# Kernel tuning notes

Measured on AMD Instinct MI355X. Metric: run time of the kernel, lower is better.

## Reference

```python
import jax, jax.numpy as jnp
import numpy as np

T = 1024          # tokens (flattened batch*seq)
H = 1024          # hidden_size
NH = 8            # num_attention_heads
NKV = 4           # num_key_value_heads
HD = H // NH      # head_dim = 128
E = 32            # n_routed_experts
TOPK = 4          # num_experts_per_tok
NG = 8            # n_group
TKG = 4           # topk_group
MI = 512          # moe_intermediate_size
SI = MI * 2       # shared experts intermediate (n_shared_experts=2)
THETA = 10000.0
EPS = 1e-6
RSF = 2.5         # routed_scaling_factor


def setup_inputs() -> dict:
    key = jax.random.key(0)
    ks = jax.random.split(key, 16)
    s = jnp.float32(0.02)
    def nrm(k, shape):
        return jax.random.normal(k, shape, jnp.float32) * s
    return {
        "hidden_states": jax.random.normal(ks[0], (T, H), jnp.float32),
        "position_ids": jnp.arange(T, dtype=jnp.int32),
        "ln1_w": jnp.ones((H,), jnp.float32),
        "ln2_w": jnp.ones((H,), jnp.float32),
        "q_w": nrm(ks[1], (H, H)),            # torch Linear layout [out, in]
        "k_w": nrm(ks[2], (NKV * HD, H)),
        "v_w": nrm(ks[3], (NKV * HD, H)),
        "o_w": nrm(ks[4], (H, H)),
        "router_w": nrm(ks[5], (E, H)),
        "router_bias": jnp.zeros((E,), jnp.float32),  # e_score_correction_bias
        "eg_w": nrm(ks[6], (E, H, MI)),       # expert gate_proj, [E, in, out]
        "eu_w": nrm(ks[7], (E, H, MI)),       # expert up_proj
        "ed_w": nrm(ks[8], (E, MI, H)),       # expert down_proj
        "sg_w": nrm(ks[9], (H, SI)),          # shared experts gate_proj, [in, out]
        "su_w": nrm(ks[10], (H, SI)),
        "sd_w": nrm(ks[11], (SI, H)),
    }


def rmsnorm(x, w):
    var = jnp.mean(x * x, axis=-1, keepdims=True)
    return x * jax.lax.rsqrt(var + EPS) * w


def apply_rope(x, pos):
    # x: [T, heads, HD], non-interleaved (half-rotation)
    half = HD // 2
    inv_freq = 1.0 / (THETA ** (jnp.arange(half, dtype=jnp.float32) / half))
    freqs = pos.astype(jnp.float32)[:, None] * inv_freq[None, :]  # [T, half]
    cos = jnp.cos(freqs)[:, None, :]
    sin = jnp.sin(freqs)[:, None, :]
    x1, x2 = x[..., :half], x[..., half:]
    return jnp.concatenate([x1 * cos - x2 * sin, x2 * cos + x1 * sin], axis=-1)


def attention(h, pos, q_w, k_w, v_w, o_w):
    q = (h @ q_w.T).reshape(T, NH, HD)
    k = (h @ k_w.T).reshape(T, NKV, HD)
    v = (h @ v_w.T).reshape(T, NKV, HD)
    q = apply_rope(q, pos)
    k = apply_rope(k, pos)
    rep = NH // NKV
    k = jnp.repeat(k, rep, axis=1)  # [T, NH, HD]
    v = jnp.repeat(v, rep, axis=1)
    scale = 1.0 / np.sqrt(HD).astype(np.float32)
    scores = jnp.einsum("qhd,khd->hqk", q, k) * scale  # [NH, T, T]
    causal = jnp.tril(jnp.ones((T, T), bool))
    scores = jnp.where(causal[None], scores, jnp.finfo(scores.dtype).min)
    probs = jax.nn.softmax(scores, axis=-1)
    out = jnp.einsum("hqk,khd->qhd", probs, v).reshape(T, H)
    return out @ o_w.T


def router(x, router_w, router_bias):
    logits = x.astype(jnp.float32) @ router_w.T  # [T, E]
    scores = jax.nn.sigmoid(logits)
    sfc = scores + router_bias[None, :]
    # group-limited routing: sum of top-2 per group
    group_scores = jax.lax.top_k(sfc.reshape(T, NG, E // NG), 2)[0].sum(-1)  # [T, NG]
    gidx = jax.lax.top_k(group_scores, TKG)[1]  # [T, TKG]
    gmask = jnp.zeros((T, NG), jnp.float32).at[jnp.arange(T)[:, None], gidx].set(1.0)
    smask = jnp.repeat(gmask, E // NG, axis=1) > 0  # [T, E]
    masked = jnp.where(smask, sfc, 0.0)
    topk_idx = jax.lax.top_k(masked, TOPK)[1]  # [T, TOPK]
    topk_w = jnp.take_along_axis(scores, topk_idx, axis=1)
    topk_w = topk_w / (topk_w.sum(-1, keepdims=True) + 1e-20)  # norm_topk_prob
    return topk_idx, topk_w * RSF


def moe(x, router_w, router_bias, eg_w, eu_w, ed_w, sg_w, su_w, sd_w):
    topk_idx, topk_w = router(x, router_w, router_bias)
    # combine weights [T, E]
    cw = jnp.zeros((T, E), jnp.float32).at[jnp.arange(T)[:, None], topk_idx].add(topk_w)
    g = jnp.einsum("th,ehi->eti", x, eg_w)
    u = jnp.einsum("th,ehi->eti", x, eu_w)
    a = jax.nn.silu(g) * u
    o = jnp.einsum("eti,eih->eth", a, ed_w)
    routed = jnp.einsum("eth,te->th", o, cw)
    shared = (jax.nn.silu(x @ sg_w) * (x @ su_w)) @ sd_w
    return routed + shared


def reference(hidden_states, position_ids, ln1_w, ln2_w, q_w, k_w, v_w, o_w,
              router_w, router_bias, eg_w, eu_w, ed_w, sg_w, su_w, sd_w):
    res = hidden_states
    h = rmsnorm(hidden_states, ln1_w)
    h = attention(h, position_ids, q_w, k_w, v_w, o_w)
    h = res + h
    res = h
    h = rmsnorm(h, ln2_w)
    h = moe(h, router_w, router_bias, eg_w, eu_w, ed_w, sg_w, su_w, sd_w)
    return h + res
```

## Files before the change

### kernel.cpp

```cpp
#include <hip/hip_runtime.h>
#include <math.h>

#define T 1024
#define H 1024
#define NH 8
#define NKV 4
#define HD 128
#define NE 32
#define TOPK 4
#define NG 8
#define MI 512
#define SI 1024
#define RSF 2.5f
#define EPS 1e-6f

#define ASPLIT 4
#define SPLITK 256
#define NPSLOT 40

#define KP 40

typedef short bf16x8 __attribute__((ext_vector_type(8)));
typedef float f32x4 __attribute__((ext_vector_type(4)));
#define MFMA16(a, b, c) __builtin_amdgcn_mfma_f32_16x16x32_bf16((a), (b), (c), 0, 0, 0)

__device__ inline unsigned short f2bf(float x) {
    unsigned u = __float_as_uint(x);
    u += 0x7fff + ((u >> 16) & 1);
    return (unsigned short)(u >> 16);
}
__device__ inline float bf2f(unsigned short h) { return __uint_as_float(((unsigned)h) << 16); }

__device__ __host__ inline int cqb_of(int qb) {
    int a = qb >> 2, r = qb & 3;
    return (a + 1) * (2 * a + r);
}

union U16S {
    unsigned short s[16];
    uint4 q[2];
};

__device__ __forceinline__ void gl16(const void* g, void* l) {
    __builtin_amdgcn_global_load_lds((const __attribute__((address_space(1))) unsigned int*)g,
                                     (__attribute__((address_space(3))) unsigned int*)l, 16, 0, 0);
}

__global__ void rmsnorm_split_kernel(const float* __restrict__ x, const float* __restrict__ w,
                                     unsigned short* __restrict__ oh,
                                     unsigned short* __restrict__ ol) {
    int t = blockIdx.x;
    __shared__ float red[256];
    const float* xr = x + (size_t)t * H;
    float s = 0.f;
    for (int i = threadIdx.x; i < H; i += 256) { float v = xr[i]; s += v * v; }
    red[threadIdx.x] = s;
    __syncthreads();
    for (int st = 128; st > 0; st >>= 1) {
        if (threadIdx.x < st) red[threadIdx.x] += red[threadIdx.x + st];
        __syncthreads();
    }
    float inv = rsqrtf(red[0] / (float)H + EPS);
    for (int i = threadIdx.x; i < H; i += 256) {
        float v = xr[i] * inv * w[i];
        unsigned short hb = f2bf(v);
        oh[(size_t)t * H + i] = hb;
        ol[(size_t)t * H + i] = f2bf(v - bf2f(hb));
    }
}

__global__ void rmsnorm_dual_kernel(const float* __restrict__ x, const float* __restrict__ w,
                                    float* __restrict__ outf, unsigned short* __restrict__ outb) {
    int t = blockIdx.x;
    __shared__ float red[256];
    const float* xr = x + (size_t)t * H;
    float s = 0.f;
    for (int i = threadIdx.x; i < H; i += 256) { float v = xr[i]; s += v * v; }
    red[threadIdx.x] = s;
    __syncthreads();
// ... 104 lines not shown
    *(uint4*)&VTl[drow] = ol.q[0];
    *(uint4*)&VTl[drow + 8] = ol.q[1];
}

__global__ __launch_bounds__(256) void router_logits_kernel(const float* __restrict__ x,
                                                            const float* __restrict__ W,
                                                            float* __restrict__ logits) {
    int t = blockIdx.x;
    __shared__ float xs[H];
    int tid = threadIdx.x;
    *(float4*)&xs[tid * 4] = *(const float4*)&x[(size_t)t * H + tid * 4];
    __syncthreads();
    int e = tid >> 3, p = tid & 7;
    const float* wr = W + (size_t)e * H;
    float s = 0.f;
#pragma unroll
    for (int i = 0; i < 32; ++i) {
        int k = i * 32 + p * 4;
        float4 wv = *(const float4*)&wr[k];
        float4 xv = *(const float4*)&xs[k];
        s += wv.x * xv.x + wv.y * xv.y + wv.z * xv.z + wv.w * xv.w;
    }
#pragma unroll
    for (int off = 1; off < 8; off <<= 1) s += __shfl_xor(s, off);
    if (p == 0) logits[(size_t)t * NE + e] = s;
}

__global__ __launch_bounds__(256) void gemm3_qkv(
    const unsigned short* __restrict__ Xh, const unsigned short* __restrict__ Xl,
    const unsigned short* __restrict__ Wqh, const unsigned short* __restrict__ Wql,
    const unsigned short* __restrict__ Wkh, const unsigned short* __restrict__ Wkl,
    const unsigned short* __restrict__ Wvh, const unsigned short* __restrict__ Wvl,
    float* __restrict__ qo, float* __restrict__ ko, float* __restrict__ vo) {
    __shared__ short Ahs[2][128][32], Als[2][128][32], Bhs[2][64][32], Bls[2][64][32];
    int tid = threadIdx.x;
    int m0 = blockIdx.y * 128;
    int n0 = blockIdx.x * 64;
    const unsigned short *Wh, *Wl;
    float* O;
    int ldo, nc0;
    if (n0 < 1024) { nc0 = n0; Wh = Wqh; Wl = Wql; O = qo; ldo = H; }
    else if (n0 < 1536) { nc0 = n0 - 1024; Wh = Wkh; Wl = Wkl; O = ko; ldo = NKV * HD; }
    else { nc0 = n0 - 1536; Wh = Wvh; Wl = Wvl; O = vo; ldo = NKV * HD; }
    int wave = tid >> 6, lane = tid & 63;
    int lr = lane & 15, lq = lane >> 4;
    int wm = (wave >> 1) * 64, wn = (wave & 1) * 32;
    int srow = lane >> 2, skb = (lane & 3) * 8;
    const unsigned short *ah_p[2], *al_p[2];
#pragma unroll
    for (int p = 0; p < 2; ++p) {
        int m = m0 + wave * 32 + p * 16 + srow;
        ah_p[p] = Xh + (size_t)m * H + skb;
        al_p[p] = Xl + (size_t)m * H + skb;
    }
    int bn = nc0 + wave * 16 + srow;
    const unsigned short* bh_p = Wh + (size_t)bn * H + skb;
    const unsigned short* bl_p = Wl + (size_t)bn * H + skb;
    f32x4 acc[4][2];
#pragma unroll
    for (int i = 0; i < 4; ++i)
#pragma unroll
        for (int j = 0; j < 2; ++j) acc[i][j] = (f32x4){0.f, 0.f, 0.f, 0.f};
    for (int k0 = 0; k0 < H; k0 += 64) {
#pragma unroll
        for (int c = 0; c < 2; ++c) {
            int kc = k0 + c * 32;
#pragma unroll
            for (int p = 0; p < 2; ++p) {
                gl16(ah_p[p] + kc, &Ahs[c][wave * 32 + p * 16 + srow][skb]);
                gl16(al_p[p] + kc, &Als[c][wave * 32 + p * 16 + srow][skb]);
            }
            gl16(bh_p + kc, &Bhs[c][wave * 16 + srow][skb]);
            gl16(bl_p + kc, &Bls[c][wave * 16 + srow][skb]);
        }
        __syncthreads();
#pragma unroll
        for (int c = 0; c < 2; ++c) {
            bf16x8 a_h[4], a_l[4], b_h[2], b_l[2];
#pragma unroll
            for (int mt = 0; mt < 4; ++mt) {
                a_h[mt] = *(const bf16x8*)&Ahs[c][wm + mt * 16 + lr][lq * 8];
                a_l[mt] = *(const bf16x8*)&Als[c][wm + mt * 16 + lr][lq * 8];
            }
#pragma unroll
            for (int nt = 0; nt < 2; ++nt) {
                b_h[nt] = *(const bf16x8*)&Bhs[c][wn + nt * 16 + lr][lq * 8];
                b_l[nt] = *(const bf16x8*)&Bls[c][wn + nt * 16 + lr][lq * 8];
            }
#pragma unroll
            for (int mt = 0; mt < 4; ++mt)
#pragma unroll
                for (int nt = 0; nt < 2; ++nt) {
                    acc[mt][nt] = MFMA16(a_h[mt], b_h[nt], acc[mt][nt]);
                    acc[mt][nt] = MFMA16(a_h[mt], b_l[nt], acc[mt][nt]);
                    acc[mt][nt] = MFMA16(a_l[mt], b_h[nt], acc[mt][nt]);
                }
        }
        __syncthreads();
    }
#pragma unroll
    for (int mt = 0; mt < 4; ++mt)
#pragma unroll
        for (int nt = 0; nt < 2; ++nt)
#pragma unroll
            for (int p = 0; p < 4; ++p) {
                int m = m0 + wm + mt * 16 + lq * 4 + p;
                int col = nc0 + wn + nt * 16 + lr;
                O[(size_t)m * ldo + col] = acc[mt][nt][p];
            }
}

__global__ __launch_bounds__(256) void gemm3_res(
    const unsigned short* __restrict__ Agh, const unsigned short* __restrict__ Agl,
    const unsigned short* __restrict__ Wh, const unsigned short* __restrict__ Wl,
    const float* __restrict__ res, float* __restrict__ O) {
    __shared__ short Ahs[2][128][32], Als[2][128][32], Bhs[2][64][32], Bls[2][64][32];
    int tid = threadIdx.x;
    int m0 = blockIdx.y * 128;
    int n0 = blockIdx.x * 64;
    int wave = tid >> 6, lane = tid & 63;
    int lr = lane & 15, lq = lane >> 4;
    int wm = (wave >> 1) * 64, wn = (wave & 1) * 32;
    int srow = lane >> 2, skb = (lane & 3) * 8;
    const unsigned short *ah_p[2], *al_p[2];
#pragma unroll
    for (int p = 0; p < 2; ++p) {
        int m = m0 + wave * 32 + p * 16 + srow;
        ah_p[p] = Agh + (size_t)m * H + skb;
        al_p[p] = Agl + (size_t)m * H + skb;
    }
    int bn = n0 + wave * 16 + srow;
    const unsigned short* bh_p = Wh + (size_t)bn * H + skb;
    const unsigned short* bl_p = Wl + (size_t)bn * H + skb;
    f32x4 acc[4][2];
#pragma unroll
    for (int i = 0; i < 4; ++i)
#pragma unroll
        for (int j = 0; j < 2; ++j) acc[i][j] = (f32x4){0.f, 0.f, 0.f, 0.f};
    for (int k0 = 0; k0 < H; k0 += 64) {
#pragma unroll
        for (int c = 0; c < 2; ++c) {
            int kc = k0 + c * 32;
#pragma unroll
            for (int p = 0; p < 2; ++p) {
                gl16(ah_p[p] + kc, &Ahs[c][wave * 32 + p * 16 + srow][skb]);
                gl16(al_p[p] + kc, &Als[c][wave * 32 + p * 16 + srow][skb]);
            }
            gl16(bh_p + kc, &Bhs[c][wave * 16 + srow][skb]);
            gl16(bl_p + kc, &Bls[c][wave * 16 + srow][skb]);
        }
        __syncthreads();
#pragma unroll
        for (int c = 0; c < 2; ++c) {
            bf16x8 a_h[4], a_l[4], b_h[2], b_l[2];
#pragma unroll
            for (int mt = 0; mt < 4; ++mt) {
                a_h[mt] = *(const bf16x8*)&Ahs[c][wm + mt * 16 + lr][lq * 8];
                a_l[mt] = *(const bf16x8*)&Als[c][wm + mt * 16 + lr][lq * 8];
            }
#pragma unroll
            for (int nt = 0; nt < 2; ++nt) {
                b_h[nt] = *(const bf16x8*)&Bhs[c][wn + nt * 16 + lr][lq * 8];
                b_l[nt] = *(const bf16x8*)&Bls[c][wn + nt * 16 + lr][lq * 8];
            }
#pragma unroll
            for (int mt = 0; mt < 4; ++mt)
#pragma unroll
                for (int nt = 0; nt < 2; ++nt) {
                    acc[mt][nt] = MFMA16(a_h[mt], b_h[nt], acc[mt][nt]);
                    acc[mt][nt] = MFMA16(a_h[mt], b_l[nt], acc[mt][nt]);
                    acc[mt][nt] = MFMA16(a_l[mt], b_h[nt], acc[mt][nt]);
                }
        }
        __syncthreads();
    }
#pragma unroll
    for (int mt = 0; mt < 4; ++mt)
#pragma unroll
        for (int nt = 0; nt < 2; ++nt)
#pragma unroll
            for (int p = 0; p < 4; ++p) {
                int m = m0 + wm + mt * 16 + lq * 4 + p;
                int col = n0 + wn + nt * 16 + lr;
                O[(size_t)m * H + col] = res[(size_t)m * H + col] + acc[mt][nt][p];
            }
}

__global__ void rope_kernel(float* __restrict__ q, const float* __restrict__ k,
                            const int* __restrict__ pos, unsigned short* __restrict__ Khg,
                            unsigned short* __restrict__ Klg) {
    int i = blockIdx.x * 256 + threadIdx.x;
    const int totq = T * NH * 64;
    const int tot = totq + T * NKV * 64;
    if (i >= tot) return;
    if (i < totq) {
        int r = i;
        int d = r & 63; r >>= 6;
        int hh = r % NH, t = r / NH;
        float p = (float)pos[t];
        float inv = powf(10000.0f, -(float)d / 64.0f);
        float fr = p * inv;
        float sv, cv;
        sincosf(fr, &sv, &cv);
        size_t bi = ((size_t)t * NH + hh) * HD + d;
        float x1 = q[bi], x2 = q[bi + 64];
        q[bi] = x1 * cv - x2 * sv;
        q[bi + 64] = x2 * cv + x1 * sv;
    } else {
// ... 289 lines not shown

__global__ void bucket_kernel(const int* __restrict__ topk_idx, int* __restrict__ counts,
                              int* __restrict__ offs, int* __restrict__ tok_of,
                              int* __restrict__ slot_of) {
    __shared__ int cnt[NE], off[NE], fil[NE];
    int tid = threadIdx.x;
    if (tid < NE) { cnt[tid] = 0; fil[tid] = 0; }
    __syncthreads();
    for (int i = tid; i < T * TOPK; i += 256) atomicAdd(&cnt[topk_idx[i]], 1);
    __syncthreads();
    if (tid == 0) {
        int a = 0;
        for (int e = 0; e < NE; ++e) { off[e] = a; a += cnt[e]; }
    }
    __syncthreads();
    if (tid < NE) { counts[tid] = cnt[tid]; offs[tid] = off[tid]; }
    for (int i = tid; i < T * TOPK; i += 256) {
        int e = topk_idx[i];
        int p = off[e] + atomicAdd(&fil[e], 1);
        tok_of[p] = i >> 2;
        slot_of[i] = p;
    }
}

__global__ __launch_bounds__(256) void up_mfma2(
    const unsigned short* __restrict__ Xb, const unsigned short* __restrict__ Gt,
    const unsigned short* __restrict__ Ut, size_t wstride, const int* __restrict__ tok_of,
    const int* __restrict__ offs, const int* __restrict__ counts, int eoff,
    unsigned short* __restrict__ outb, int ldo) {
    int zl = blockIdx.z;
    int e = eoff + zl;
    int cnt = counts ? counts[e] : T;
    int base = offs ? offs[e] : 0;
    int m0 = blockIdx.y * 128;
    if (m0 >= cnt) return;
    int n0 = blockIdx.x * 64;
    const unsigned short* gt = Gt + (size_t)zl * wstride;
    const unsigned short* ut = Ut + (size_t)zl * wstride;
    __shared__ __attribute__((aligned(16))) short As[2][128][KP];
    __shared__ __attribute__((aligned(16))) short Gs[2][64][KP];
    __shared__ __attribute__((aligned(16))) short Us[2][64][KP];
    __shared__ int toks[128];
    int tid = threadIdx.x;
    if (tid < 128) {
        int m = m0 + tid;
        if (m >= cnt) m = cnt - 1;
        toks[tid] = tok_of ? tok_of[base + m] : m;
    }
    __syncthreads();
    int wave = tid >> 6, lane = tid & 63;
    int lr = lane & 15, lq = lane >> 4;
    int wm = (wave >> 1) * 64, wn = (wave & 1) * 32;
    int srow = lane >> 2, skb = (lane & 3) * 8;
    const unsigned short* aptr[2];
#pragma unroll
    for (int p = 0; p < 2; ++p)
        aptr[p] = Xb + (size_t)toks[wave * 32 + p * 16 + srow] * H + skb;
    const unsigned short* gptr = gt + (size_t)(n0 + wave * 16 + srow) * H + skb;
    const unsigned short* uptr = ut + (size_t)(n0 + wave * 16 + srow) * H + skb;
    f32x4 ag[4][2], au[4][2];
#pragma unroll
    for (int i = 0; i < 4; ++i)
#pragma unroll
        for (int j = 0; j < 2; ++j) {
            ag[i][j] = (f32x4){0.f, 0.f, 0.f, 0.f};
            au[i][j] = (f32x4){0.f, 0.f, 0.f, 0.f};
        }
    uint4 ra00, ra01, ra10, ra11, rg0, rg1, ru0, ru1;
#define LOADU(K0)                                          \
    {                                                      \
        ra00 = *(const uint4*)(aptr[0] + (K0));            \
        ra01 = *(const uint4*)(aptr[1] + (K0));            \
        ra10 = *(const uint4*)(aptr[0] + (K0) + 32);       \
        ra11 = *(const uint4*)(aptr[1] + (K0) + 32);       \
        rg0 = *(const uint4*)(gptr + (K0));                \
        rg1 = *(const uint4*)(gptr + (K0) + 32);           \
        ru0 = *(const uint4*)(uptr + (K0));                \
        ru1 = *(const uint4*)(uptr + (K0) + 32);           \
    }
    LOADU(0);
    for (int k0 = 0; k0 < H; k0 += 64) {
        __syncthreads();
        *(uint4*)&As[0][wave * 32 + srow][skb] = ra00;
        *(uint4*)&As[0][wave * 32 + 16 + srow][skb] = ra01;
        *(uint4*)&As[1][wave * 32 + srow][skb] = ra10;
        *(uint4*)&As[1][wave * 32 + 16 + srow][skb] = ra11;
        *(uint4*)&Gs[0][wave * 16 + srow][skb] = rg0;
        *(uint4*)&Gs[1][wave * 16 + srow][skb] = rg1;
        *(uint4*)&Us[0][wave * 16 + srow][skb] = ru0;
        *(uint4*)&Us[1][wave * 16 + srow][skb] = ru1;
        __syncthreads();
        if (k0 + 64 < H) LOADU(k0 + 64);
#pragma unroll
        for (int c = 0; c < 2; ++c) {
            bf16x8 a[4], gg[2], uu[2];
#pragma unroll
            for (int mt = 0; mt < 4; ++mt)
                a[mt] = *(const bf16x8*)&As[c][wm + mt * 16 + lr][lq * 8];
#pragma unroll
            for (int nt = 0; nt < 2; ++nt) {
                gg[nt] = *(const bf16x8*)&Gs[c][wn + nt * 16 + lr][lq * 8];
                uu[nt] = *(const bf16x8*)&Us[c][wn + nt * 16 + lr][lq * 8];
            }
#pragma unroll
            for (int mt = 0; mt < 4; ++mt)
#pragma unroll
                for (int nt = 0; nt < 2; ++nt) {
                    ag[mt][nt] = MFMA16(a[mt], gg[nt], ag[mt][nt]);
                    au[mt][nt] = MFMA16(a[mt], uu[nt], au[mt][nt]);
                }
        }
    }
#undef LOADU
#pragma unroll
    for (int mt = 0; mt < 4; ++mt)
#pragma unroll
        for (int nt = 0; nt < 2; ++nt)
#pragma unroll
            for (int p = 0; p < 4; ++p) {
                int m = m0 + wm + mt * 16 + lq * 4 + p;
                if (m >= cnt) continue;
                int orow = tok_of ? base + m : m;
                int col = n0 + wn + nt * 16 + lr;
                float gv = ag[mt][nt][p], uv = au[mt][nt][p];
                float sv = gv / (1.f + __expf(-gv)) * uv;
                outb[(size_t)orow * ldo + col] = f2bf(sv);
            }
}

__global__ __launch_bounds__(256) void down_mfma2(const unsigned short* __restrict__ Ab, int K,
                                                  const unsigned short* __restrict__ Wt,
                                                  size_t wstride, const int* __restrict__ offs,
                                                  const int* __restrict__ counts, int eoff,
                                                  float* __restrict__ Co) {
    int zl = blockIdx.z;
    int e = eoff + zl;
    int cnt = counts ? counts[e] : T;
    int base = offs ? offs[e] : 0;
    int m0 = blockIdx.y * 128;
    if (m0 >= cnt) return;
    int n0 = blockIdx.x * 128;
    const unsigned short* wt = Wt + (size_t)zl * wstride;
    __shared__ __attribute__((aligned(16))) short As[2][128][KP];
    __shared__ __attribute__((aligned(16))) short Bs[2][128][KP];
    int tid = threadIdx.x;
    int wave = tid >> 6, lane = tid & 63;
    int lr = lane & 15, lq = lane >> 4;
    int wm = (wave >> 1) * 64, wn = (wave & 1) * 64;
    int srow = lane >> 2, skb = (lane & 3) * 8;
    const unsigned short* aptr[2];
    const unsigned short* bptr[2];
#pragma unroll
    for (int p = 0; p < 2; ++p) {
        int m = m0 + wave * 32 + p * 16 + srow;
        if (m >= cnt) m = cnt - 1;
        aptr[p] = Ab + (size_t)(base + m) * K + skb;
        bptr[p] = wt + (size_t)(n0 + wave * 32 + p * 16 + srow) * K + skb;
    }
    f32x4 acc[4][4];
#pragma unroll
    for (int i = 0; i < 4; ++i)
#pragma unroll
        for (int j = 0; j < 4; ++j) acc[i][j] = (f32x4){0.f, 0.f, 0.f, 0.f};
    uint4 ra00, ra01, ra10, ra11, rb00, rb01, rb10, rb11;
#define LOADD(K0)                                          \
    {                                                      \
        ra00 = *(const uint4*)(aptr[0] + (K0));            \
        ra01 = *(const uint4*)(aptr[1] + (K0));            \
        ra10 = *(const uint4*)(aptr[0] + (K0) + 32);       \
        ra11 = *(const uint4*)(aptr[1] + (K0) + 32);       \
        rb00 = *(const uint4*)(bptr[0] + (K0));            \
        rb01 = *(const uint4*)(bptr[1] + (K0));            \
        rb10 = *(const uint4*)(bptr[0] + (K0) + 32);       \
        rb11 = *(const uint4*)(bptr[1] + (K0) + 32);       \
    }
    LOADD(0);
    for (int k0 = 0; k0 < K; k0 += 64) {
        __syncthreads();
        *(uint4*)&As[0][wave * 32 + srow][skb] = ra00;
        *(uint4*)&As[0][wave * 32 + 16 + srow][skb] = ra01;
        *(uint4*)&As[1][wave * 32 + srow][skb] = ra10;
        *(uint4*)&As[1][wave * 32 + 16 + srow][skb] = ra11;
        *(uint4*)&Bs[0][wave * 32 + srow][skb] = rb00;
        *(uint4*)&Bs[0][wave * 32 + 16 + srow][skb] = rb01;
        *(uint4*)&Bs[1][wave * 32 + srow][skb] = rb10;
        *(uint4*)&Bs[1][wave * 32 + 16 + srow][skb] = rb11;
        __syncthreads();
        if (k0 + 64 < K) LOADD(k0 + 64);
#pragma unroll
        for (int c = 0; c < 2; ++c) {
            bf16x8 a[4], b[4];
#pragma unroll
            for (int mt = 0; mt < 4; ++mt)
                a[mt] = *(const bf16x8*)&As[c][wm + mt * 16 + lr][lq * 8];
#pragma unroll
            for (int nt = 0; nt < 4; ++nt)
                b[nt] = *(const bf16x8*)&Bs[c][wn + nt * 16 + lr][lq * 8];
#pragma unroll
            for (int mt = 0; mt < 4; ++mt)
#pragma unroll
                for (int nt = 0; nt < 4; ++nt) acc[mt][nt] = MFMA16(a[mt], b[nt], acc[mt][nt]);
        }
    }
#undef LOADD
#pragma unroll
    for (int mt = 0; mt < 4; ++mt)
#pragma unroll
        for (int nt = 0; nt < 4; ++nt)
#pragma unroll
            for (int p = 0; p < 4; ++p) {
                int m = m0 + wm + mt * 16 + lq * 4 + p;
                if (m >= cnt) continue;
                int col = n0 + wn + nt * 16 + lr;
                Co[(size_t)(base + m) * H + col] = acc[mt][nt][p];
            }
}

__global__ void combine_kernel(const float* __restrict__ o_slot, const int* __restrict__ slot_of,
                               const float* __restrict__ topkw, const float* __restrict__ h2,
                               const float* __restrict__ sharedo, float* __restrict__ out) {
    int t = blockIdx.x;
    int d = threadIdx.x * 4;
    float4 a = *(const float4*)&h2[(size_t)t * H + d];
    float4 b = *(const float4*)&sharedo[(size_t)t * H + d];
    float4 acc = make_float4(a.x + b.x, a.y + b.y, a.z + b.z, a.w + b.w);
#pragma unroll
    for (int r = 0; r < TOPK; ++r) {
        int s = slot_of[t * TOPK + r];
        float w = topkw[t * TOPK + r];
        float4 v = *(const float4*)&o_slot[(size_t)s * H + d];
        acc.x += w * v.x; acc.y += w * v.y; acc.z += w * v.z; acc.w += w * v.w;
    }
    *(float4*)&out[(size_t)t * H + d] = acc;
}

extern "C" void kernel_launch(void* const* d_in, const int* in_sizes, int n_in,
                              void* d_out, int out_size, void* d_ws, size_t ws_size,
// ... 76 lines not shown
    unsigned short* egT = arena;
    unsigned short* euT = arena + (size_t)16 * H * MI;
    unsigned short* edT = arena;
    unsigned short* sgT = arena;
    unsigned short* suT = arena + (size_t)H * SI;
    unsigned short* sdT = arena;

    dim3 b256(256);

    split_w4<<<dim3(HH / (256 * 4), 1, 4), b256, 0, stream>>>(q_w, k_w, v_w, o_w, Wqh, Wql,
                                                              Wkh, Wkl, Wvh, Wvl, Woh, Wol);
    rmsnorm_split_kernel<<<T, b256, 0, stream>>>(hidden, ln1w, Xh, Xl);

    gemm3_qkv<<<dim3(32, 8), b256, 0, stream>>>(Xh, Xl, Wqh, Wql, Wkh, Wkl, Wvh, Wvl,
                                                qb, kb, vb);
    {
        int tot = T * NH * 64 + T * NKV * 64;
        rope_kernel<<<(tot + 255) / 256, b256, 0, stream>>>(qb, kb, pos, Khg, Klg);
    }
    vt_split<<<dim3(T / 64, (NKV * HD) / 64), b256, 0, stream>>>(vb, VTh, VTl);
    attn_split<<<dim3(NH, T / 64, ASPLIT), b256, 0, stream>>>(qb, Khg, Klg, VTh, VTl,
                                                              attn_po, attn_pm, attn_pl);
    attn_merge<<<dim3(NH, T / 64), b256, 0, stream>>>(attn_po, attn_pm, attn_pl, Aoh, Aol);
    gemm3_res<<<dim3(16, 8), b256, 0, stream>>>(Aoh, Aol, Woh, Wol, hidden, h2);
    rmsnorm_dual_kernel<<<T, b256, 0, stream>>>(h2, ln2w, h_ln2f, h_ln2b);

    router_logits_kernel<<<T, b256, 0, stream>>>(h_ln2f, router_w, logits);
    router_kernel<<<(T + 255) / 256, b256, 0, stream>>>(logits, router_b, topk_idx, topkw);
    bucket_kernel<<<1, b256, 0, stream>>>(topk_idx, counts, offs, tok_of, slot_of);

    if (big_ws) {
        transpose_cvt<<<dim3(MI / 64, H / 64, NE), b256, 0, stream>>>(eg_w, egTall, H, MI, 0);
        transpose_cvt<<<dim3(MI / 64, H / 64, NE), b256, 0, stream>>>(eu_w, euTall, H, MI, 0);
        up_mfma2<<<dim3(MI / 64, 8, NE), b256, 0, stream>>>(
            h_ln2b, egTall, euTall, (size_t)H * MI, tok_of, offs, counts, 0, abuf, MI);
        transpose_cvt<<<dim3(H / 64, MI / 64, NE), b256, 0, stream>>>(ed_w, edTall, MI, H, 0);
        down_mfma2<<<dim3(H / 128, 8, NE), b256, 0, stream>>>(
            abuf, MI, edTall, (size_t)MI * H, offs, counts, 0, o_slot);
    } else {
        for (int g = 0; g < 2; ++g) {
            int eo = g * 16;
            transpose_cvt<<<dim3(MI / 64, H / 64, 16), b256, 0, stream>>>(eg_w, egT, H, MI, eo);
            transpose_cvt<<<dim3(MI / 64, H / 64, 16), b256, 0, stream>>>(eu_w, euT, H, MI, eo);
            up_mfma2<<<dim3(MI / 64, 8, 16), b256, 0, stream>>>(
                h_ln2b, egT, euT, (size_t)H * MI, tok_of, offs, counts, eo, abuf, MI);
        }
        for (int g = 0; g < 2; ++g) {
            int eo = g * 16;
            transpose_cvt<<<dim3(H / 64, MI / 64, 16), b256, 0, stream>>>(ed_w, edT, MI, H, eo);
            down_mfma2<<<dim3(H / 128, 8, 16), b256, 0, stream>>>(
                abuf, MI, edT, (size_t)MI * H, offs, counts, eo, o_slot);
        }
    }
    transpose_cvt<<<dim3(SI / 64, H / 64, 1), b256, 0, stream>>>(sg_w, sgT, H, SI, 0);
    transpose_cvt<<<dim3(SI / 64, H / 64, 1), b256, 0, stream>>>(su_w, suT, H, SI, 0);
    up_mfma2<<<dim3(SI / 64, T / 128, 1), b256, 0, stream>>>(
        h_ln2b, sgT, suT, 0, nullptr, nullptr, nullptr, 0, ashared, SI);
    transpose_cvt<<<dim3(H / 64, SI / 64, 1), b256, 0, stream>>>(sd_w, sdT, SI, H, 0);
    down_mfma2<<<dim3(H / 128, T / 128, 1), b256, 0, stream>>>(
        ashared, SI, sdT, 0, nullptr, nullptr, 0, sharedo);

    combine_kernel<<<T, b256, 0, stream>>>(o_slot, slot_of, topkw, h2, sharedo, out);
}
```

Before: 517.8 us.

## Register-prefetch QKV/res GEMMs and double register prefetch in MoE GEMMs

The QKV and residual GEMMs drop direct global-to-LDS loads in favour of register-staged prefetching of the next K tile, with padded LDS rows (KP) to reduce bank conflicts. The routed up/down expert GEMMs gain a second register buffer so loads run two tiles ahead of the MFMA work. The aim is to hide global memory latency behind compute, at the cost of higher VGPR use that may reduce occupancy.

```diff
diff --git a/kernel.cpp b/kernel.cpp
--- a/kernel.cpp
+++ b/kernel.cpp
@@ -40,11 +40,6 @@
     unsigned short s[16];
     uint4 q[2];
 };
-
-__device__ __forceinline__ void gl16(const void* g, void* l) {
-    __builtin_amdgcn_global_load_lds((const __attribute__((address_space(1))) unsigned int*)g,
-                                     (__attribute__((address_space(3))) unsigned int*)l, 16, 0, 0);
-}
 
 __global__ void rmsnorm_split_kernel(const float* __restrict__ x, const float* __restrict__ w,
                                      unsigned short* __restrict__ oh,
@@ -215,7 +210,8 @@
     const unsigned short* __restrict__ Wkh, const unsigned short* __restrict__ Wkl,
     const unsigned short* __restrict__ Wvh, const unsigned short* __restrict__ Wvl,
     float* __restrict__ qo, float* __restrict__ ko, float* __restrict__ vo) {
-    __shared__ short Ahs[2][128][32], Als[2][128][32], Bhs[2][64][32], Bls[2][64][32];
+    __shared__ __attribute__((aligned(16))) short Ahs[2][128][KP], Als[2][128][KP];
+    __shared__ __attribute__((aligned(16))) short Bhs[2][64][KP], Bls[2][64][KP];
     int tid = threadIdx.x;
     int m0 = blockIdx.y * 128;
     int n0 = blockIdx.x * 64;
@@ -244,19 +240,39 @@
     for (int i = 0; i < 4; ++i)
 #pragma unroll
         for (int j = 0; j < 2; ++j) acc[i][j] = (f32x4){0.f, 0.f, 0.f, 0.f};
+    uint4 rah0, rah1, rah2, rah3, ral0, ral1, ral2, ral3, rbh0, rbh1, rbl0, rbl1;
+#define LOADQ(K0)                                              \
+    {                                                          \
+        rah0 = *(const uint4*)(ah_p[0] + (K0));                \
+        rah1 = *(const uint4*)(ah_p[1] + (K0));                \
+        rah2 = *(const uint4*)(ah_p[0] + (K0) + 32);           \
+        rah3 = *(const uint4*)(ah_p[1] + (K0) + 32);           \
+        ral0 = *(const uint4*)(al_p[0] + (K0));                \
+        ral1 = *(const uint4*)(al_p[1] + (K0));                \
+        ral2 = *(const uint4*)(al_p[0] + (K0) + 32);           \
+        ral3 = *(const uint4*)(al_p[1] + (K0) + 32);           \
+        rbh0 = *(const uint4*)(bh_p + (K0));                   \
+        rbh1 = *(const uint4*)(bh_p + (K0) + 32);              \
+        rbl0 = *(const uint4*)(bl_p + (K0));                   \
+        rbl1 = *(const uint4*)(bl_p + (K0) + 32);              \
+    }
+    LOADQ(0);
     for (int k0 = 0; k0 < H; k0 += 64) {
-#pragma unroll
-        for (int c = 0; c < 2; ++c) {
-            int kc = k0 + c * 32;
-#pragma unroll
-            for (int p = 0; p < 2; ++p) {
-                gl16(ah_p[p] + kc, &Ahs[c][wave * 32 + p * 16 + srow][skb]);
-                gl16(al_p[p] + kc, &Als[c][wave * 32 + p * 16 + srow][skb]);
-            }
-            gl16(bh_p + kc, &Bhs[c][wave * 16 + srow][skb]);
-            gl16(bl_p + kc, &Bls[c][wave * 16 + srow][skb]);
-        }
-        __syncthreads();
+        __syncthreads();
+        *(uint4*)&Ahs[0][wave * 32 + srow][skb] = rah0;
+        *(uint4*)&Ahs[0][wave * 32 + 16 + srow][skb] = rah1;
+        *(uint4*)&Ahs[1][wave * 32 + srow][skb] = rah2;
+        *(uint4*)&Ahs[1][wave * 32 + 16 + srow][skb] = rah3;
+        *(uint4*)&Als[0][wave * 32 + srow][skb] = ral0;
+        *(uint4*)&Als[0][wave * 32 + 16 + srow][skb] = ral1;
+        *(uint4*)&Als[1][wave * 32 + srow][skb] = ral2;
+        *(uint4*)&Als[1][wave * 32 + 16 + srow][skb] = ral3;
+        *(uint4*)&Bhs[0][wave * 16 + srow][skb] = rbh0;
+        *(uint4*)&Bhs[1][wave * 16 + srow][skb] = rbh1;
+        *(uint4*)&Bls[0][wave * 16 + srow][skb] = rbl0;
+        *(uint4*)&Bls[1][wave * 16 + srow][skb] = rbl1;
+        __syncthreads();
+        if (k0 + 64 < H) LOADQ(k0 + 64);
 #pragma unroll
         for (int c = 0; c < 2; ++c) {
             bf16x8 a_h[4], a_l[4], b_h[2], b_l[2];
@@ -279,8 +295,8 @@
                     acc[mt][nt] = MFMA16(a_l[mt], b_h[nt], acc[mt][nt]);
                 }
         }
-        __syncthreads();
-    }
+    }
+#undef LOADQ
 #pragma unroll
     for (int mt = 0; mt < 4; ++mt)
 #pragma unroll
@@ -297,7 +313,8 @@
     const unsigned short* __restrict__ Agh, const unsigned short* __restrict__ Agl,
     const unsigned short* __restrict__ Wh, const unsigned short* __restrict__ Wl,
     const float* __restrict__ res, float* __restrict__ O) {
-    __shared__ short Ahs[2][128][32], Als[2][128][32], Bhs[2][64][32], Bls[2][64][32];
+    __shared__ __attribute__((aligned(16))) short Ahs[2][128][KP], Als[2][128][KP];
+    __shared__ __attribute__((aligned(16))) short Bhs[2][64][KP], Bls[2][64][KP];
     int tid = threadIdx.x;
     int m0 = blockIdx.y * 128;
     int n0 = blockIdx.x * 64;
@@ -320,19 +337,39 @@
     for (int i = 0; i < 4; ++i)
 #pragma unroll
         for (int j = 0; j < 2; ++j) acc[i][j] = (f32x4){0.f, 0.f, 0.f, 0.f};
+    uint4 rah0, rah1, rah2, rah3, ral0, ral1, ral2, ral3, rbh0, rbh1, rbl0, rbl1;
+#define LOADR(K0)                                              \
+    {                                                          \
+        rah0 = *(const uint4*)(ah_p[0] + (K0));                \
+        rah1 = *(const uint4*)(ah_p[1] + (K0));                \
+        rah2 = *(const uint4*)(ah_p[0] + (K0) + 32);           \
+        rah3 = *(const uint4*)(ah_p[1] + (K0) + 32);           \
+        ral0 = *(const uint4*)(al_p[0] + (K0));                \
+        ral1 = *(const uint4*)(al_p[1] + (K0));                \
+        ral2 = *(const uint4*)(al_p[0] + (K0) + 32);           \
+        ral3 = *(const uint4*)(al_p[1] + (K0) + 32);           \
+        rbh0 = *(const uint4*)(bh_p + (K0));                   \
+        rbh1 = *(const uint4*)(bh_p + (K0) + 32);              \
+        rbl0 = *(const uint4*)(bl_p + (K0));                   \
+        rbl1 = *(const uint4*)(bl_p + (K0) + 32);              \
+    }
+    LOADR(0);
     for (int k0 = 0; k0 < H; k0 += 64) {
-#pragma unroll
-        for (int c = 0; c < 2; ++c) {
-            int kc = k0 + c * 32;
-#pragma unroll
-            for (int p = 0; p < 2; ++p) {
-                gl16(ah_p[p] + kc, &Ahs[c][wave * 32 + p * 16 + srow][skb]);
-                gl16(al_p[p] + kc, &Als[c][wave * 32 + p * 16 + srow][skb]);
-            }
-            gl16(bh_p + kc, &Bhs[c][wave * 16 + srow][skb]);
-            gl16(bl_p + kc, &Bls[c][wave * 16 + srow][skb]);
-        }
-        __syncthreads();
+        __syncthreads();
+        *(uint4*)&Ahs[0][wave * 32 + srow][skb] = rah0;
+        *(uint4*)&Ahs[0][wave * 32 + 16 + srow][skb] = rah1;
+        *(uint4*)&Ahs[1][wave * 32 + srow][skb] = rah2;
+        *(uint4*)&Ahs[1][wave * 32 + 16 + srow][skb] = rah3;
+        *(uint4*)&Als[0][wave * 32 + srow][skb] = ral0;
+        *(uint4*)&Als[0][wave * 32 + 16 + srow][skb] = ral1;
+        *(uint4*)&Als[1][wave * 32 + srow][skb] = ral2;
+        *(uint4*)&Als[1][wave * 32 + 16 + srow][skb] = ral3;
+        *(uint4*)&Bhs[0][wave * 16 + srow][skb] = rbh0;
+        *(uint4*)&Bhs[1][wave * 16 + srow][skb] = rbh1;
+        *(uint4*)&Bls[0][wave * 16 + srow][skb] = rbl0;
+        *(uint4*)&Bls[1][wave * 16 + srow][skb] = rbl1;
+        __syncthreads();
+        if (k0 + 64 < H) LOADR(k0 + 64);
 #pragma unroll
         for (int c = 0; c < 2; ++c) {
             bf16x8 a_h[4], a_l[4], b_h[2], b_l[2];
@@ -355,8 +392,8 @@
                     acc[mt][nt] = MFMA16(a_l[mt], b_h[nt], acc[mt][nt]);
                 }
         }
-        __syncthreads();
-    }
+    }
+#undef LOADR
 #pragma unroll
     for (int mt = 0; mt < 4; ++mt)
 #pragma unroll
@@ -747,7 +784,8 @@
             au[i][j] = (f32x4){0.f, 0.f, 0.f, 0.f};
         }
     uint4 ra00, ra01, ra10, ra11, rg0, rg1, ru0, ru1;
-#define LOADU(K0)                                          \
+    uint4 sa00, sa01, sa10, sa11, sg0, sg1, su0, su1;
+#define LOADUA(K0)                                         \
     {                                                      \
         ra00 = *(const uint4*)(aptr[0] + (K0));            \
         ra01 = *(const uint4*)(aptr[1] + (K0));            \
@@ -758,8 +796,37 @@
         ru0 = *(const uint4*)(uptr + (K0));                \
         ru1 = *(const uint4*)(uptr + (K0) + 32);           \
     }
-    LOADU(0);
-    for (int k0 = 0; k0 < H; k0 += 64) {
+#define LOADUB(K0)                                         \
+    {                                                      \
+        sa00 = *(const uint4*)(aptr[0] + (K0));            \
+        sa01 = *(const uint4*)(aptr[1] + (K0));            \
+        sa10 = *(const uint4*)(aptr[0] + (K0) + 32);       \
+        sa11 = *(const uint4*)(aptr[1] + (K0) + 32);       \
+        sg0 = *(const uint4*)(gptr + (K0));                \
+        sg1 = *(const uint4*)(gptr + (K0) + 32);           \
+        su0 = *(const uint4*)(uptr + (K0));                \
+        su1 = *(const uint4*)(uptr + (K0) + 32);           \
+    }
+#define UPMMA                                                                     \
+    {                                                                             \
+        _Pragma("unroll") for (int c = 0; c < 2; ++c) {                           \
+            bf16x8 a[4], gg[2], uu[2];                                            \
+            _Pragma("unroll") for (int mt = 0; mt < 4; ++mt)                      \
+                a[mt] = *(const bf16x8*)&As[c][wm + mt * 16 + lr][lq * 8];        \
+            _Pragma("unroll") for (int nt = 0; nt < 2; ++nt) {                    \
+                gg[nt] = *(const bf16x8*)&Gs[c][wn + nt * 16 + lr][lq * 8];       \
+                uu[nt] = *(const bf16x8*)&Us[c][wn + nt * 16 + lr][lq * 8];       \
+            }                                                                     \
+            _Pragma("unroll") for (int mt = 0; mt < 4; ++mt)                      \
+                _Pragma("unroll") for (int nt = 0; nt < 2; ++nt) {                \
+                    ag[mt][nt] = MFMA16(a[mt], gg[nt], ag[mt][nt]);               \
+                    au[mt][nt] = MFMA16(a[mt], uu[nt], au[mt][nt]);               \
+                }                                                                 \
+        }                                                                         \
+    }
+    LOADUA(0);
+    LOADUB(64);
+    for (int k0 = 0; k0 < H; k0 += 128) {
         __syncthreads();
         *(uint4*)&As[0][wave * 32 + srow][skb] = ra00;
         *(uint4*)&As[0][wave * 32 + 16 + srow][skb] = ra01;
@@ -770,28 +837,24 @@
         *(uint4*)&Us[0][wave * 16 + srow][skb] = ru0;
         *(uint4*)&Us[1][wave * 16 + srow][skb] = ru1;
         __syncthreads();
-        if (k0 + 64 < H) LOADU(k0 + 64);
-#pragma unroll
-        for (int c = 0; c < 2; ++c) {
-            bf16x8 a[4], gg[2], uu[2];
-#pragma unroll
-            for (int mt = 0; mt < 4; ++mt)
-                a[mt] = *(const bf16x8*)&As[c][wm + mt * 16 + lr][lq * 8];
-#pragma unroll
-            for (int nt = 0; nt < 2; ++nt) {
-                gg[nt] = *(const bf16x8*)&Gs[c][wn + nt * 16 + lr][lq * 8];
-                uu[nt] = *(const bf16x8*)&Us[c][wn + nt * 16 + lr][lq * 8];
-            }
-#pragma unroll
-            for (int mt = 0; mt < 4; ++mt)
-#pragma unroll
-                for (int nt = 0; nt < 2; ++nt) {
-                    ag[mt][nt] = MFMA16(a[mt], gg[nt], ag[mt][nt]);
-                    au[mt][nt] = MFMA16(a[mt], uu[nt], au[mt][nt]);
-                }
-        }
-    }
-#undef LOADU
+        if (k0 + 128 < H) LOADUA(k0 + 128);
+        UPMMA;
+        __syncthreads();
+        *(uint4*)&As[0][wave * 32 + srow][skb] = sa00;
+        *(uint4*)&As[0][wave * 32 + 16 + srow][skb] = sa01;
+        *(uint4*)&As[1][wave * 32 + srow][skb] = sa10;
+        *(uint4*)&As[1][wave * 32 + 16 + srow][skb] = sa11;
+        *(uint4*)&Gs[0][wave * 16 + srow][skb] = sg0;
+        *(uint4*)&Gs[1][wave * 16 + srow][skb] = sg1;
+        *(uint4*)&Us[0][wave * 16 + srow][skb] = su0;
+        *(uint4*)&Us[1][wave * 16 + srow][skb] = su1;
+        __syncthreads();
+        if (k0 + 192 < H) LOADUB(k0 + 192);
+        UPMMA;
+    }
+#undef LOADUA
+#undef LOADUB
+#undef UPMMA
 #pragma unroll
     for (int mt = 0; mt < 4; ++mt)
 #pragma unroll
@@ -843,7 +906,8 @@
 #pragma unroll
         for (int j = 0; j < 4; ++j) acc[i][j] = (f32x4){0.f, 0.f, 0.f, 0.f};
     uint4 ra00, ra01, ra10, ra11, rb00, rb01, rb10, rb11;
-#define LOADD(K0)                                          \
+    uint4 sa00, sa01, sa10, sa11, sb00, sb01, sb10, sb11;
+#define LOADDA(K0)                                         \
     {                                                      \
         ra00 = *(const uint4*)(aptr[0] + (K0));            \
         ra01 = *(const uint4*)(aptr[1] + (K0));            \
@@ -854,8 +918,33 @@
         rb10 = *(const uint4*)(bptr[0] + (K0) + 32);       \
         rb11 = *(const uint4*)(bptr[1] + (K0) + 32);       \
     }
-    LOADD(0);
-    for (int k0 = 0; k0 < K; k0 += 64) {
+#define LOADDB(K0)                                         \
+    {                                                      \
+        sa00 = *(const uint4*)(aptr[0] + (K0));            \
+        sa01 = *(const uint4*)(aptr[1] + (K0));            \
+        sa10 = *(const uint4*)(aptr[0] + (K0) + 32);       \
+        sa11 = *(const uint4*)(aptr[1] + (K0) + 32);       \
+        sb00 = *(const uint4*)(bptr[0] + (K0));            \
+        sb01 = *(const uint4*)(bptr[1] + (K0));            \
+        sb10 = *(const uint4*)(bptr[0] + (K0) + 32);       \
+        sb11 = *(const uint4*)(bptr[1] + (K0) + 32);       \
+    }
+#define DNMMA                                                                     \
+    {                                                                             \
+        _Pragma("unroll") for (int c = 0; c < 2; ++c) {                           \
+            bf16x8 a[4], b[4];                                                    \
+            _Pragma("unroll") for (int mt = 0; mt < 4; ++mt)                      \
+                a[mt] = *(const bf16x8*)&As[c][wm + mt * 16 + lr][lq * 8];        \
+            _Pragma("unroll") for (int nt = 0; nt < 4; ++nt)                      \
+                b[nt] = *(const bf16x8*)&Bs[c][wn + nt * 16 + lr][lq * 8];        \
+            _Pragma("unroll") for (int mt = 0; mt < 4; ++mt)                      \
+                _Pragma("unroll") for (int nt = 0; nt < 4; ++nt)                  \
+                    acc[mt][nt] = MFMA16(a[mt], b[nt], acc[mt][nt]);              \
+        }                                                                         \
+    }
+    LOADDA(0);
+    LOADDB(64);
+    for (int k0 = 0; k0 < K; k0 += 128) {
         __syncthreads();
         *(uint4*)&As[0][wave * 32 + srow][skb] = ra00;
         *(uint4*)&As[0][wave * 32 + 16 + srow][skb] = ra01;
@@ -866,23 +955,24 @@
         *(uint4*)&Bs[1][wave * 32 + srow][skb] = rb10;
         *(uint4*)&Bs[1][wave * 32 + 16 + srow][skb] = rb11;
         __syncthreads();
-        if (k0 + 64 < K) LOADD(k0 + 64);
-#pragma unroll
-        for (int c = 0; c < 2; ++c) {
-            bf16x8 a[4], b[4];
-#pragma unroll
-            for (int mt = 0; mt < 4; ++mt)
-                a[mt] = *(const bf16x8*)&As[c][wm + mt * 16 + lr][lq * 8];
-#pragma unroll
-            for (int nt = 0; nt < 4; ++nt)
-                b[nt] = *(const bf16x8*)&Bs[c][wn + nt * 16 + lr][lq * 8];
-#pragma unroll
-            for (int mt = 0; mt < 4; ++mt)
-#pragma unroll
-                for (int nt = 0; nt < 4; ++nt) acc[mt][nt] = MFMA16(a[mt], b[nt], acc[mt][nt]);
-        }
-    }
-#undef LOADD
+        if (k0 + 128 < K) LOADDA(k0 + 128);
+        DNMMA;
+        __syncthreads();
+        *(uint4*)&As[0][wave * 32 + srow][skb] = sa00;
+        *(uint4*)&As[0][wave * 32 + 16 + srow][skb] = sa01;
+        *(uint4*)&As[1][wave * 32 + srow][skb] = sa10;
+        *(uint4*)&As[1][wave * 32 + 16 + srow][skb] = sa11;
+        *(uint4*)&Bs[0][wave * 32 + srow][skb] = sb00;
+        *(uint4*)&Bs[0][wave * 32 + 16 + srow][skb] = sb01;
+        *(uint4*)&Bs[1][wave * 32 + srow][skb] = sb10;
+        *(uint4*)&Bs[1][wave * 32 + 16 + srow][skb] = sb11;
+        __syncthreads();
+        if (k0 + 192 < K) LOADDB(k0 + 192);
+        DNMMA;
+    }
+#undef LOADDA
+#undef LOADDB
+#undef DNMMA
 #pragma unroll
     for (int mt = 0; mt < 4; ++mt)
 #pragma unroll
```

Result: no change. 525.1 us (+1.4%).

## Register-prefetch pipeline for attention GEMMs and shrink up-projection M tile

Applied to the files above, without the earlier changes.

The QKV and output-projection GEMMs switch from direct global-to-LDS loads with a full sync per step to a register prefetch: the next K-slice is loaded into registers while MFMAs run on the current LDS tile, and the LDS rows are padded to KP columns to cut bank conflicts. Separately, the expert and shared up-projection kernel uses a 64-row M tile instead of 128, with the grid resized to match. This gives more, smaller blocks and less wasted work on sparsely filled experts. The cost is more register pressure from the prefetch buffers and less reuse of the weight tiles per block.

```diff
diff --git a/kernel.cpp b/kernel.cpp
--- a/kernel.cpp
+++ b/kernel.cpp
@@ -40,11 +40,6 @@
     unsigned short s[16];
     uint4 q[2];
 };
-
-__device__ __forceinline__ void gl16(const void* g, void* l) {
-    __builtin_amdgcn_global_load_lds((const __attribute__((address_space(1))) unsigned int*)g,
-                                     (__attribute__((address_space(3))) unsigned int*)l, 16, 0, 0);
-}
 
 __global__ void rmsnorm_split_kernel(const float* __restrict__ x, const float* __restrict__ w,
                                      unsigned short* __restrict__ oh,
@@ -215,7 +210,8 @@
     const unsigned short* __restrict__ Wkh, const unsigned short* __restrict__ Wkl,
     const unsigned short* __restrict__ Wvh, const unsigned short* __restrict__ Wvl,
     float* __restrict__ qo, float* __restrict__ ko, float* __restrict__ vo) {
-    __shared__ short Ahs[2][128][32], Als[2][128][32], Bhs[2][64][32], Bls[2][64][32];
+    __shared__ __attribute__((aligned(16))) short Ahs[2][128][KP], Als[2][128][KP];
+    __shared__ __attribute__((aligned(16))) short Bhs[2][64][KP], Bls[2][64][KP];
     int tid = threadIdx.x;
     int m0 = blockIdx.y * 128;
     int n0 = blockIdx.x * 64;
@@ -244,19 +240,39 @@
     for (int i = 0; i < 4; ++i)
 #pragma unroll
         for (int j = 0; j < 2; ++j) acc[i][j] = (f32x4){0.f, 0.f, 0.f, 0.f};
+    uint4 rah0, rah1, rah2, rah3, ral0, ral1, ral2, ral3, rbh0, rbh1, rbl0, rbl1;
+#define LOADQ(K0)                                              \
+    {                                                          \
+        rah0 = *(const uint4*)(ah_p[0] + (K0));                \
+        rah1 = *(const uint4*)(ah_p[1] + (K0));                \
+        rah2 = *(const uint4*)(ah_p[0] + (K0) + 32);           \
+        rah3 = *(const uint4*)(ah_p[1] + (K0) + 32);           \
+        ral0 = *(const uint4*)(al_p[0] + (K0));                \
+        ral1 = *(const uint4*)(al_p[1] + (K0));                \
+        ral2 = *(const uint4*)(al_p[0] + (K0) + 32);           \
+        ral3 = *(const uint4*)(al_p[1] + (K0) + 32);           \
+        rbh0 = *(const uint4*)(bh_p + (K0));                   \
+        rbh1 = *(const uint4*)(bh_p + (K0) + 32);              \
+        rbl0 = *(const uint4*)(bl_p + (K0));                   \
+        rbl1 = *(const uint4*)(bl_p + (K0) + 32);              \
+    }
+    LOADQ(0);
     for (int k0 = 0; k0 < H; k0 += 64) {
-#pragma unroll
-        for (int c = 0; c < 2; ++c) {
-            int kc = k0 + c * 32;
-#pragma unroll
-            for (int p = 0; p < 2; ++p) {
-                gl16(ah_p[p] + kc, &Ahs[c][wave * 32 + p * 16 + srow][skb]);
-                gl16(al_p[p] + kc, &Als[c][wave * 32 + p * 16 + srow][skb]);
-            }
-            gl16(bh_p + kc, &Bhs[c][wave * 16 + srow][skb]);
-            gl16(bl_p + kc, &Bls[c][wave * 16 + srow][skb]);
-        }
-        __syncthreads();
+        __syncthreads();
+        *(uint4*)&Ahs[0][wave * 32 + srow][skb] = rah0;
+        *(uint4*)&Ahs[0][wave * 32 + 16 + srow][skb] = rah1;
+        *(uint4*)&Ahs[1][wave * 32 + srow][skb] = rah2;
+        *(uint4*)&Ahs[1][wave * 32 + 16 + srow][skb] = rah3;
+        *(uint4*)&Als[0][wave * 32 + srow][skb] = ral0;
+        *(uint4*)&Als[0][wave * 32 + 16 + srow][skb] = ral1;
+        *(uint4*)&Als[1][wave * 32 + srow][skb] = ral2;
+        *(uint4*)&Als[1][wave * 32 + 16 + srow][skb] = ral3;
+        *(uint4*)&Bhs[0][wave * 16 + srow][skb] = rbh0;
+        *(uint4*)&Bhs[1][wave * 16 + srow][skb] = rbh1;
+        *(uint4*)&Bls[0][wave * 16 + srow][skb] = rbl0;
+        *(uint4*)&Bls[1][wave * 16 + srow][skb] = rbl1;
+        __syncthreads();
+        if (k0 + 64 < H) LOADQ(k0 + 64);
 #pragma unroll
         for (int c = 0; c < 2; ++c) {
             bf16x8 a_h[4], a_l[4], b_h[2], b_l[2];
@@ -279,8 +295,8 @@
                     acc[mt][nt] = MFMA16(a_l[mt], b_h[nt], acc[mt][nt]);
                 }
         }
-        __syncthreads();
-    }
+    }
+#undef LOADQ
 #pragma unroll
     for (int mt = 0; mt < 4; ++mt)
 #pragma unroll
@@ -297,7 +313,8 @@
     const unsigned short* __restrict__ Agh, const unsigned short* __restrict__ Agl,
     const unsigned short* __restrict__ Wh, const unsigned short* __restrict__ Wl,
     const float* __restrict__ res, float* __restrict__ O) {
-    __shared__ short Ahs[2][128][32], Als[2][128][32], Bhs[2][64][32], Bls[2][64][32];
+    __shared__ __attribute__((aligned(16))) short Ahs[2][128][KP], Als[2][128][KP];
+    __shared__ __attribute__((aligned(16))) short Bhs[2][64][KP], Bls[2][64][KP];
     int tid = threadIdx.x;
     int m0 = blockIdx.y * 128;
     int n0 = blockIdx.x * 64;
@@ -320,19 +337,39 @@
     for (int i = 0; i < 4; ++i)
 #pragma unroll
         for (int j = 0; j < 2; ++j) acc[i][j] = (f32x4){0.f, 0.f, 0.f, 0.f};
+    uint4 rah0, rah1, rah2, rah3, ral0, ral1, ral2, ral3, rbh0, rbh1, rbl0, rbl1;
+#define LOADR(K0)                                              \
+    {                                                          \
+        rah0 = *(const uint4*)(ah_p[0] + (K0));                \
+        rah1 = *(const uint4*)(ah_p[1] + (K0));                \
+        rah2 = *(const uint4*)(ah_p[0] + (K0) + 32);           \
+        rah3 = *(const uint4*)(ah_p[1] + (K0) + 32);           \
+        ral0 = *(const uint4*)(al_p[0] + (K0));                \
+        ral1 = *(const uint4*)(al_p[1] + (K0));                \
+        ral2 = *(const uint4*)(al_p[0] + (K0) + 32);           \
+        ral3 = *(const uint4*)(al_p[1] + (K0) + 32);           \
+        rbh0 = *(const uint4*)(bh_p + (K0));                   \
+        rbh1 = *(const uint4*)(bh_p + (K0) + 32);              \
+        rbl0 = *(const uint4*)(bl_p + (K0));                   \
+        rbl1 = *(const uint4*)(bl_p + (K0) + 32);              \
+    }
+    LOADR(0);
     for (int k0 = 0; k0 < H; k0 += 64) {
-#pragma unroll
-        for (int c = 0; c < 2; ++c) {
-            int kc = k0 + c * 32;
-#pragma unroll
-            for (int p = 0; p < 2; ++p) {
-                gl16(ah_p[p] + kc, &Ahs[c][wave * 32 + p * 16 + srow][skb]);
-                gl16(al_p[p] + kc, &Als[c][wave * 32 + p * 16 + srow][skb]);
-            }
-            gl16(bh_p + kc, &Bhs[c][wave * 16 + srow][skb]);
-            gl16(bl_p + kc, &Bls[c][wave * 16 + srow][skb]);
-        }
-        __syncthreads();
+        __syncthreads();
+        *(uint4*)&Ahs[0][wave * 32 + srow][skb] = rah0;
+        *(uint4*)&Ahs[0][wave * 32 + 16 + srow][skb] = rah1;
+        *(uint4*)&Ahs[1][wave * 32 + srow][skb] = rah2;
+        *(uint4*)&Ahs[1][wave * 32 + 16 + srow][skb] = rah3;
+        *(uint4*)&Als[0][wave * 32 + srow][skb] = ral0;
+        *(uint4*)&Als[0][wave * 32 + 16 + srow][skb] = ral1;
+        *(uint4*)&Als[1][wave * 32 + srow][skb] = ral2;
+        *(uint4*)&Als[1][wave * 32 + 16 + srow][skb] = ral3;
+        *(uint4*)&Bhs[0][wave * 16 + srow][skb] = rbh0;
+        *(uint4*)&Bhs[1][wave * 16 + srow][skb] = rbh1;
+        *(uint4*)&Bls[0][wave * 16 + srow][skb] = rbl0;
+        *(uint4*)&Bls[1][wave * 16 + srow][skb] = rbl1;
+        __syncthreads();
+        if (k0 + 64 < H) LOADR(k0 + 64);
 #pragma unroll
         for (int c = 0; c < 2; ++c) {
             bf16x8 a_h[4], a_l[4], b_h[2], b_l[2];
@@ -355,8 +392,8 @@
                     acc[mt][nt] = MFMA16(a_l[mt], b_h[nt], acc[mt][nt]);
                 }
         }
-        __syncthreads();
-    }
+    }
+#undef LOADR
 #pragma unroll
     for (int mt = 0; mt < 4; ++mt)
 #pragma unroll
@@ -712,17 +749,17 @@
     int e = eoff + zl;
     int cnt = counts ? counts[e] : T;
     int base = offs ? offs[e] : 0;
-    int m0 = blockIdx.y * 128;
+    int m0 = blockIdx.y * 64;
     if (m0 >= cnt) return;
     int n0 = blockIdx.x * 64;
     const unsigned short* gt = Gt + (size_t)zl * wstride;
     const unsigned short* ut = Ut + (size_t)zl * wstride;
-    __shared__ __attribute__((aligned(16))) short As[2][128][KP];
+    __shared__ __attribute__((aligned(16))) short As[2][64][KP];
     __shared__ __attribute__((aligned(16))) short Gs[2][64][KP];
     __shared__ __attribute__((aligned(16))) short Us[2][64][KP];
-    __shared__ int toks[128];
+    __shared__ int toks[64];
     int tid = threadIdx.x;
-    if (tid < 128) {
+    if (tid < 64) {
         int m = m0 + tid;
         if (m >= cnt) m = cnt - 1;
         toks[tid] = tok_of ? tok_of[base + m] : m;
@@ -730,52 +767,47 @@
     __syncthreads();
     int wave = tid >> 6, lane = tid & 63;
     int lr = lane & 15, lq = lane >> 4;
-    int wm = (wave >> 1) * 64, wn = (wave & 1) * 32;
-    int srow = lane >> 2, skb = (lane & 3) * 8;
-    const unsigned short* aptr[2];
-#pragma unroll
-    for (int p = 0; p < 2; ++p)
-        aptr[p] = Xb + (size_t)toks[wave * 32 + p * 16 + srow] * H + skb;
-    const unsigned short* gptr = gt + (size_t)(n0 + wave * 16 + srow) * H + skb;
-    const unsigned short* uptr = ut + (size_t)(n0 + wave * 16 + srow) * H + skb;
-    f32x4 ag[4][2], au[4][2];
-#pragma unroll
-    for (int i = 0; i < 4; ++i)
+    int wm = (wave >> 1) * 32, wn = (wave & 1) * 32;
+    int srow = tid >> 2, sq = tid & 3;
+    int sc = sq >> 1, soff = (sq & 1) * 16;
+    int skoff = sq * 16;
+    const unsigned short* aptr = Xb + (size_t)toks[srow] * H + skoff;
+    const unsigned short* gptr = gt + (size_t)(n0 + srow) * H + skoff;
+    const unsigned short* uptr = ut + (size_t)(n0 + srow) * H + skoff;
+    f32x4 ag[2][2], au[2][2];
+#pragma unroll
+    for (int i = 0; i < 2; ++i)
 #pragma unroll
         for (int j = 0; j < 2; ++j) {
             ag[i][j] = (f32x4){0.f, 0.f, 0.f, 0.f};
             au[i][j] = (f32x4){0.f, 0.f, 0.f, 0.f};
         }
-    uint4 ra00, ra01, ra10, ra11, rg0, rg1, ru0, ru1;
-#define LOADU(K0)                                          \
-    {                                                      \
-        ra00 = *(const uint4*)(aptr[0] + (K0));            \
-        ra01 = *(const uint4*)(aptr[1] + (K0));            \
-        ra10 = *(const uint4*)(aptr[0] + (K0) + 32);       \
-        ra11 = *(const uint4*)(aptr[1] + (K0) + 32);       \
-        rg0 = *(const uint4*)(gptr + (K0));                \
-        rg1 = *(const uint4*)(gptr + (K0) + 32);           \
-        ru0 = *(const uint4*)(uptr + (K0));                \
-        ru1 = *(const uint4*)(uptr + (K0) + 32);           \
+    uint4 ra0, ra1, rg0, rg1, ru0, ru1;
+#define LOADU(K0)                                      \
+    {                                                  \
+        ra0 = *(const uint4*)(aptr + (K0));            \
+        ra1 = *(const uint4*)(aptr + (K0) + 8);        \
+        rg0 = *(const uint4*)(gptr + (K0));            \
+        rg1 = *(const uint4*)(gptr + (K0) + 8);        \
+        ru0 = *(const uint4*)(uptr + (K0));            \
+        ru1 = *(const uint4*)(uptr + (K0) + 8);        \
     }
     LOADU(0);
     for (int k0 = 0; k0 < H; k0 += 64) {
         __syncthreads();
-        *(uint4*)&As[0][wave * 32 + srow][skb] = ra00;
-        *(uint4*)&As[0][wave * 32 + 16 + srow][skb] = ra01;
-        *(uint4*)&As[1][wave * 32 + srow][skb] = ra10;
-        *(uint4*)&As[1][wave * 32 + 16 + srow][skb] = ra11;
-        *(uint4*)&Gs[0][wave * 16 + srow][skb] = rg0;
-        *(uint4*)&Gs[1][wave * 16 + srow][skb] = rg1;
-        *(uint4*)&Us[0][wave * 16 + srow][skb] = ru0;
-        *(uint4*)&Us[1][wave * 16 + srow][skb] = ru1;
+        *(uint4*)&As[sc][srow][soff] = ra0;
+        *(uint4*)&As[sc][srow][soff + 8] = ra1;
+        *(uint4*)&Gs[sc][srow][soff] = rg0;
+        *(uint4*)&Gs[sc][srow][soff + 8] = rg1;
+        *(uint4*)&Us[sc][srow][soff] = ru0;
+        *(uint4*)&Us[sc][srow][soff + 8] = ru1;
         __syncthreads();
         if (k0 + 64 < H) LOADU(k0 + 64);
 #pragma unroll
         for (int c = 0; c < 2; ++c) {
-            bf16x8 a[4], gg[2], uu[2];
-#pragma unroll
-            for (int mt = 0; mt < 4; ++mt)
+            bf16x8 a[2], gg[2], uu[2];
+#pragma unroll
+            for (int mt = 0; mt < 2; ++mt)
                 a[mt] = *(const bf16x8*)&As[c][wm + mt * 16 + lr][lq * 8];
 #pragma unroll
             for (int nt = 0; nt < 2; ++nt) {
@@ -783,7 +815,7 @@
                 uu[nt] = *(const bf16x8*)&Us[c][wn + nt * 16 + lr][lq * 8];
             }
 #pragma unroll
-            for (int mt = 0; mt < 4; ++mt)
+            for (int mt = 0; mt < 2; ++mt)
 #pragma unroll
                 for (int nt = 0; nt < 2; ++nt) {
                     ag[mt][nt] = MFMA16(a[mt], gg[nt], ag[mt][nt]);
@@ -793,7 +825,7 @@
     }
 #undef LOADU
 #pragma unroll
-    for (int mt = 0; mt < 4; ++mt)
+    for (int mt = 0; mt < 2; ++mt)
 #pragma unroll
         for (int nt = 0; nt < 2; ++nt)
 #pragma unroll
@@ -1025,7 +1057,7 @@
     if (big_ws) {
         transpose_cvt<<<dim3(MI / 64, H / 64, NE), b256, 0, stream>>>(eg_w, egTall, H, MI, 0);
         transpose_cvt<<<dim3(MI / 64, H / 64, NE), b256, 0, stream>>>(eu_w, euTall, H, MI, 0);
-        up_mfma2<<<dim3(MI / 64, 8, NE), b256, 0, stream>>>(
+        up_mfma2<<<dim3(MI / 64, T / 64, NE), b256, 0, stream>>>(
             h_ln2b, egTall, euTall, (size_t)H * MI, tok_of, offs, counts, 0, abuf, MI);
         transpose_cvt<<<dim3(H / 64, MI / 64, NE), b256, 0, stream>>>(ed_w, edTall, MI, H, 0);
         down_mfma2<<<dim3(H / 128, 8, NE), b256, 0, stream>>>(
@@ -1035,7 +1067,7 @@
             int eo = g * 16;
             transpose_cvt<<<dim3(MI / 64, H / 64, 16), b256, 0, stream>>>(eg_w, egT, H, MI, eo);
             transpose_cvt<<<dim3(MI / 64, H / 64, 16), b256, 0, stream>>>(eu_w, euT, H, MI, eo);
-            up_mfma2<<<dim3(MI / 64, 8, 16), b256, 0, stream>>>(
+            up_mfma2<<<dim3(MI / 64, T / 64, 16), b256, 0, stream>>>(
                 h_ln2b, egT, euT, (size_t)H * MI, tok_of, offs, counts, eo, abuf, MI);
         }
         for (int g = 0; g < 2; ++g) {
@@ -1047,7 +1079,7 @@
     }
     transpose_cvt<<<dim3(SI / 64, H / 64, 1), b256, 0, stream>>>(sg_w, sgT, H, SI, 0);
     transpose_cvt<<<dim3(SI / 64, H / 64, 1), b256, 0, stream>>>(su_w, suT, H, SI, 0);
-    up_mfma2<<<dim3(SI / 64, T / 128, 1), b256, 0, stream>>>(
+    up_mfma2<<<dim3(SI / 64, T / 64, 1), b256, 0, stream>>>(
         h_ln2b, sgT, suT, 0, nullptr, nullptr, nullptr, 0, ashared, SI);
     transpose_cvt<<<dim3(H / 64, SI / 64, 1), b256, 0, stream>>>(sd_w, sdT, SI, H, 0);
     down_mfma2<<<dim3(H / 128, T / 128, 1), b256, 0, stream>>>(
```

Measured after the change: 485.1 us. -6.3%, faster.
